# Kernel tuning notes

Measured on AMD Instinct MI355X. Metric: run time of the kernel, lower is better.

The kernel has to match this reference:

```python
import jax, jax.numpy as jnp
import numpy as np

B, N, F, T = 32, 1024, 64, 24


def setup_inputs() -> dict:
    key = jax.random.key(0)
    k = jax.random.split(key, 6)
    x = jax.random.normal(k[0], (B, N, F, T), dtype=jnp.float32)
    W1 = jax.random.normal(k[1], (T,), dtype=jnp.float32) * 0.1
    W2 = jax.random.normal(k[2], (F, T), dtype=jnp.float32) * 0.1
    W3 = jax.random.normal(k[3], (F,), dtype=jnp.float32) * 0.1
    b_s = jax.random.normal(k[4], (1, N, N), dtype=jnp.float32) * 0.02
    V_s = jax.random.normal(k[5], (N, N), dtype=jnp.float32) * 0.02
    return {"x": x, "W1": W1, "W2": W2, "W3": W3, "b_s": b_s, "V_s": V_s}


def reference(x, W1, W2, W3, b_s, V_s):
    # lhs = (x @ W1) @ W2 : (B,N,F,T)@(T,) -> (B,N,F) ; @(F,T) -> (B,N,T)
    lhs = jnp.einsum('bnft,t->bnf', x, W1) @ W2
    # rhs = (x^T @ W3) permuted : (B,N,T,F)@(F,) -> (B,N,T) -> (B,T,N)
    rhs = jnp.einsum('bnft,f->btn', x, W3)
    # batch_dot: (B,N,T) @ (B,T,N) -> (B,N,N), as one batched GEMM
    product = jnp.einsum('bnt,btm->bnm', lhs, rhs)
    sig = jax.nn.sigmoid(product + b_s)
    # torch.matmul(V_s, sig.permute(1,2,0)).permute(2,0,1) == S[b,n,i] = sum_k V_s[i,k]*sig[b,n,k]
    S = jnp.einsum('ik,bnk->bni', V_s, sig)
    S = S - jnp.max(S, axis=1, keepdims=True)
    exp = jnp.exp(S)
    # NOTE: original has `[0]` on the sum -> denominator uses batch-0 sums, shape (1,N),
    # broadcast over rows. Faithfully reproduced (numpy broadcasting matches torch here).
    return exp / jnp.sum(exp, axis=1, keepdims=True)[0]
```

## Files before the change

### kernel.cpp

```cpp
#include <hip/hip_runtime.h>
#include <hip/hip_bf16.h>

#define Bb 32
#define Nn 1024
#define Ff 64
#define Tt 24

#define LHS_OFF  0
#define RHS_OFF  3145728
#define MKEY_OFF 6291456
#define D0_OFF   6422528
#define ABF_OFF  6426624ull
#define VB_OFF   73535488ull
#define WS_NEED  75632640ull

typedef __attribute__((ext_vector_type(8))) short bf16x8;
typedef __attribute__((ext_vector_type(4))) float f32x4;

__device__ __forceinline__ unsigned fkey(float x) {
    unsigned u = __float_as_uint(x);
    return (u & 0x80000000u) ? ~u : (u | 0x80000000u);
}
__device__ __forceinline__ float keyToFloat(unsigned k) {
    unsigned u = (k & 0x80000000u) ? (k & 0x7FFFFFFFu) : ~k;
    return __uint_as_float(u);
}
__device__ __forceinline__ unsigned short f2bf(float f) {
    unsigned u = __float_as_uint(f);
    u += 0x7FFFu + ((u >> 16) & 1u);
    return (unsigned short)(u >> 16);
}

__global__ __launch_bounds__(256) void k1_lhs_rhs(
    const float* __restrict__ x, const float* __restrict__ W1,
    const float* __restrict__ W2, const float* __restrict__ W3,
    float* __restrict__ LHS, float* __restrict__ RHS) {
    __shared__ float sx[4][64][25];
    __shared__ float sy[4][64];
    __shared__ float sW1[24];
    __shared__ float sW2[64][24];
    __shared__ float sW3[64];
    int tid = threadIdx.x;
    if (tid < 24) sW1[tid] = W1[tid];
    if (tid < 64) sW3[tid] = W3[tid];
    for (int j = tid; j < 64 * 24; j += 256) sW2[j / 24][j % 24] = W2[j];
    __syncthreads();

    int w = tid >> 6, lane = tid & 63;
    int row = blockIdx.x * 4 + w;
    const float* xr = x + (size_t)row * (Ff * Tt) + lane * Tt;
    float4 xv[6];
#pragma unroll
    for (int j = 0; j < 6; ++j) xv[j] = reinterpret_cast<const float4*>(xr)[j];
    float y = 0.f;
#pragma unroll
    for (int j = 0; j < 6; ++j) {
        y += xv[j].x * sW1[j * 4 + 0] + xv[j].y * sW1[j * 4 + 1] +
             xv[j].z * sW1[j * 4 + 2] + xv[j].w * sW1[j * 4 + 3];
    }
#pragma unroll
    for (int j = 0; j < 6; ++j) {
        sx[w][lane][j * 4 + 0] = xv[j].x;
        sx[w][lane][j * 4 + 1] = xv[j].y;
        sx[w][lane][j * 4 + 2] = xv[j].z;
        sx[w][lane][j * 4 + 3] = xv[j].w;
    }
    sy[w][lane] = y;
    __syncthreads();
    if (lane < 24) {
        int t = lane;
        float la = 0.f, ra = 0.f;
#pragma unroll 8
        for (int f = 0; f < 64; ++f) {
            ra += sx[w][f][t] * sW3[f];
            la += sy[w][f] * sW2[f][t];
        }
        LHS[(size_t)row * Tt + t] = la;
        RHS[(size_t)row * Tt + t] = ra;
    }
}

__global__ __launch_bounds__(256) void k_vb(const float* __restrict__ V,
                                            unsigned* __restrict__ Vb2) {
    size_t idx = (size_t)blockIdx.x * 256 + threadIdx.x;
    float4 v = ((const float4*)V)[idx];
    uint2 o;
    o.x = (unsigned)f2bf(v.x) | ((unsigned)f2bf(v.y) << 16);
    o.y = (unsigned)f2bf(v.z) | ((unsigned)f2bf(v.w) << 16);
    ((uint2*)Vb2)[idx] = o;
}

__global__ __launch_bounds__(256) void k2a_sig(
    const float* __restrict__ LHS, const float* __restrict__ RHS,
    const float* __restrict__ b_s, unsigned short* __restrict__ Abf) {
    __shared__ float rst[24][68];
    int tid = threadIdx.x;
    int b = blockIdx.z;
    int n0 = blockIdx.x * 64;
    int kh = blockIdx.y * 512;
    int n = tid >> 2, q = tid & 3;

    float L[24];
    const float* lp = LHS + ((size_t)b * Nn + n0 + n) * Tt;
#pragma unroll
    for (int j = 0; j < 24; ++j) L[j] = lp[j];

    for (int kc = 0; kc < 512; kc += 64) {
        __syncthreads();
        const float* rp = RHS + ((size_t)b * Nn + kh + kc) * Tt;
        for (int e = tid; e < 64 * 24; e += 256) rst[e % 24][e / 24] = rp[e];
        __syncthreads();

        float P[16] = {};
#pragma unroll
        for (int j = 0; j < 24; ++j) {
            float Lj = L[j];
            const float4* rv = (const float4*)&rst[j][q * 16];
            float4 r0 = rv[0], r1 = rv[1], r2 = rv[2], r3 = rv[3];
            P[0]  += Lj * r0.x; P[1]  += Lj * r0.y; P[2]  += Lj * r0.z; P[3]  += Lj * r0.w;
            P[4]  += Lj * r1.x; P[5]  += Lj * r1.y; P[6]  += Lj * r1.z; P[7]  += Lj * r1.w;
            P[8]  += Lj * r2.x; P[9]  += Lj * r2.y; P[10] += Lj * r2.z; P[11] += Lj * r2.w;
            P[12] += Lj * r3.x; P[13] += Lj * r3.y; P[14] += Lj * r3.z; P[15] += Lj * r3.w;
        }
        const float* bp = &b_s[(size_t)(n0 + n) * Nn + kh + kc + q * 16];
        unsigned ow[8];
#pragma unroll
        for (int k4 = 0; k4 < 4; ++k4) {
            float4 bs = ((const float4*)bp)[k4];
            unsigned short s0 = f2bf(1.f / (1.f + __expf(-(P[k4 * 4 + 0] + bs.x))));
            unsigned short s1 = f2bf(1.f / (1.f + __expf(-(P[k4 * 4 + 1] + bs.y))));
            unsigned short s2 = f2bf(1.f / (1.f + __expf(-(P[k4 * 4 + 2] + bs.z))));
            unsigned short s3 = f2bf(1.f / (1.f + __expf(-(P[k4 * 4 + 3] + bs.w))));
            ow[k4 * 2 + 0] = (unsigned)s0 | ((unsigned)s1 << 16);
            ow[k4 * 2 + 1] = (unsigned)s2 | ((unsigned)s3 << 16);
        }
        unsigned short* op = Abf + ((size_t)b * Nn + n0 + n) * Nn + kh + kc + q * 16;
        ((uint4*)op)[0] = make_uint4(ow[0], ow[1], ow[2], ow[3]);
        ((uint4*)op)[1] = make_uint4(ow[4], ow[5], ow[6], ow[7]);
    }
}

__global__ __launch_bounds__(512, 2) void k2b_8ph(
    const unsigned short* __restrict__ A, const unsigned short* __restrict__ Vb,
    float* __restrict__ S, unsigned* __restrict__ Mkey) {
    __shared__ __align__(16) unsigned short lds[65536];

    const int tid = threadIdx.x, w = tid >> 6, lane = tid & 63;
    const int l15 = lane & 15;
    const int bid = blockIdx.x;
    const int L = ((bid & 7) << 6) + (bid >> 3);
    const int i0 = (L & 3) * 256;
    const int m0 = (L >> 2) * 256;
    const int wr = w >> 2, wc = w & 3;

    const int p0 = (lane >> 4) ^ ((lane >> 1) & 7);
    const int aBase  = (wr * 128 + l15) * 64 + p0 * 8;
    const int aBaseX = aBase ^ 32;
    const int bBase  = 16384 + (wc * 64 + l15) * 64 + p0 * 8;
    const int bBaseX = bBase ^ 32;

    const int rL = lane >> 3;
    const int cS = (lane & 7) ^ ((4 * (w & 1) + (lane >> 4)) & 7);
    const int bRowW = (w >> 2) * 64 + (w & 3) * 8;
    const unsigned short* srcA00 = A  + (size_t)(m0 +   0 + 8 * w + rL) * 1024 + cS * 8;
    const unsigned short* srcA01 = A  + (size_t)(m0 + 128 + 8 * w + rL) * 1024 + cS * 8;
    const unsigned short* srcA10 = A  + (size_t)(m0 +  64 + 8 * w + rL) * 1024 + cS * 8;
    const unsigned short* srcA11 = A  + (size_t)(m0 + 192 + 8 * w + rL) * 1024 + cS * 8;
    const unsigned short* srcB00 = Vb + (size_t)(i0 +   0 + bRowW + rL) * 1024 + cS * 8;
    const unsigned short* srcB01 = Vb + (size_t)(i0 + 128 + bRowW + rL) * 1024 + cS * 8;
    const unsigned short* srcB10 = Vb + (size_t)(i0 +  32 + bRowW + rL) * 1024 + cS * 8;
    const unsigned short* srcB11 = Vb + (size_t)(i0 + 160 + bRowW + rL) * 1024 + cS * 8;
    const int dA00 = (0   + 8 * w) * 64, dA01 = (128 + 8 * w) * 64;
    const int dA10 = (64  + 8 * w) * 64, dA11 = (192 + 8 * w) * 64;
    const int dB00 = 16384 + (0   + bRowW) * 64, dB01 = 16384 + (128 + bRowW) * 64;
    const int dB10 = 16384 + (32  + bRowW) * 64, dB11 = 16384 + (160 + bRowW) * 64;

#define GLD(src, dstShorts) __builtin_amdgcn_global_load_lds(                      \
        (const __attribute__((address_space(1))) void*)(src),                     \
        (__attribute__((address_space(3))) void*)(lds + (dstShorts)), 16, 0, 0)

#define READ_A(bc, mh) do {                                                        \
    const int ro_ = (bc) * 32768 + (mh) * 4096;                                    \
    aR[0][0] = *(const bf16x8*)(lds + ro_ + aBase +    0);                         \
    aR[1][0] = *(const bf16x8*)(lds + ro_ + aBase + 1024);                         \
    aR[2][0] = *(const bf16x8*)(lds + ro_ + aBase + 2048);                         \
    aR[3][0] = *(const bf16x8*)(lds + ro_ + aBase + 3072);                         \
    aR[0][1] = *(const bf16x8*)(lds + ro_ + aBaseX +    0);                        \
    aR[1][1] = *(const bf16x8*)(lds + ro_ + aBaseX + 1024);                        \
    aR[2][1] = *(const bf16x8*)(lds + ro_ + aBaseX + 2048);                        \
    aR[3][1] = *(const bf16x8*)(lds + ro_ + aBaseX + 3072);                        \
} while (0)

#define READ_B(bc, nh, BR) do {                                                    \
    const int ro_ = (bc) * 32768 + (nh) * 2048;                                    \
    BR[0][0] = *(const bf16x8*)(lds + ro_ + bBase +    0);                         \
    BR[1][0] = *(const bf16x8*)(lds + ro_ + bBase + 1024);                         \
    BR[0][1] = *(const bf16x8*)(lds + ro_ + bBaseX +    0);                        \
    BR[1][1] = *(const bf16x8*)(lds + ro_ + bBaseX + 1024);                        \
} while (0)

#define BARRIER_LGKM                                                               \
    __builtin_amdgcn_s_barrier();                                                  \
    asm volatile("s_waitcnt lgkmcnt(0)" ::: "memory");                             \
    __builtin_amdgcn_sched_barrier(0)

#define QUAD(mh, nh, BR) do {                                                      \
    __builtin_amdgcn_s_setprio(1);                                                 \
    _Pragma("unroll")                                                              \
    for (int ks_ = 0; ks_ < 2; ++ks_)                                              \
        _Pragma("unroll")                                                          \
        for (int mi_ = 0; mi_ < 4; ++mi_)                                          \
            _Pragma("unroll")                                                      \
            for (int ni_ = 0; ni_ < 2; ++ni_)                                      \
                acc[(mh) * 4 + mi_][(nh) * 2 + ni_] =                              \
                    __builtin_amdgcn_mfma_f32_16x16x32_bf16(                       \
                        aR[mi_][ks_], BR[ni_][ks_],                                \
                        acc[(mh) * 4 + mi_][(nh) * 2 + ni_], 0, 0, 0);             \
    __builtin_amdgcn_s_setprio(0);                                                 \
} while (0)

#define VM6  asm volatile("s_waitcnt vmcnt(6)" ::: "memory")
#define ENDP __builtin_amdgcn_s_barrier()

    GLD(srcA00, dA00); GLD(srcA01, dA01);
    GLD(srcB00, dB00); GLD(srcB01, dB01);
    GLD(srcB10, dB10); GLD(srcB11, dB11);
    GLD(srcA10, dA10); GLD(srcA11, dA11);
    GLD(srcA00 + 64, 32768 + dA00); GLD(srcA01 + 64, 32768 + dA01);
    GLD(srcB00 + 64, 32768 + dB00); GLD(srcB01 + 64, 32768 + dB01);
    GLD(srcB10 + 64, 32768 + dB10); GLD(srcB11 + 64, 32768 + dB11);
    asm volatile("s_waitcnt vmcnt(6)" ::: "memory");
    __builtin_amdgcn_s_barrier();

    bf16x8 aR[4][2], b0R[2][2], b1R[2][2];
    f32x4 acc[8][4] = {};

    for (int j = 0; j < 8; ++j) {
        const int k1o = (2 * j + 1) * 64;
        const int k2o = ((j < 7) ? (2 * j + 2) : 15) * 64;
        const int k3o = ((j < 7) ? (2 * j + 3) : 15) * 64;

        READ_A(0, 0); READ_B(0, 0, b0R);
        GLD(srcA10 + k1o, 32768 + dA10); GLD(srcA11 + k1o, 32768 + dA11);
        BARRIER_LGKM; QUAD(0, 0, b0R); ENDP;
        READ_B(0, 1, b1R);
        GLD(srcA00 + k2o, dA00); GLD(srcA01 + k2o, dA01);
        BARRIER_LGKM; QUAD(0, 1, b1R); ENDP;
        READ_A(0, 1);
        GLD(srcB00 + k2o, dB00); GLD(srcB01 + k2o, dB01);
        BARRIER_LGKM; QUAD(1, 0, b0R); ENDP;
        GLD(srcB10 + k2o, dB10); GLD(srcB11 + k2o, dB11);
        BARRIER_LGKM; QUAD(1, 1, b1R); VM6; ENDP;
        READ_A(1, 0); READ_B(1, 0, b0R);
        GLD(srcA10 + k2o, dA10); GLD(srcA11 + k2o, dA11);
        BARRIER_LGKM; QUAD(0, 0, b0R); ENDP;
        READ_B(1, 1, b1R);
        GLD(srcA00 + k3o, 32768 + dA00); GLD(srcA01 + k3o, 32768 + dA01);
        BARRIER_LGKM; QUAD(0, 1, b1R); ENDP;
        READ_A(1, 1);
        GLD(srcB00 + k3o, 32768 + dB00); GLD(srcB01 + k3o, 32768 + dB01);
        BARRIER_LGKM; QUAD(1, 0, b0R); ENDP;
        GLD(srcB10 + k3o, 32768 + dB10); GLD(srcB11 + k3o, 32768 + dB11);
        BARRIER_LGKM; QUAD(1, 1, b1R); VM6; ENDP;
    }
#undef GLD
#undef READ_A
#undef READ_B
#undef BARRIER_LGKM
#undef QUAD
#undef VM6
#undef ENDP

    const int ic = i0 + wc * 64 + l15;
    const int mrb = m0 + wr * 128 + (lane >> 4) * 4;
#pragma unroll
    for (int mi8 = 0; mi8 < 8; ++mi8)
#pragma unroll
        for (int ni = 0; ni < 4; ++ni) {
            f32x4 v = acc[mi8][ni];
#pragma unroll
            for (int r = 0; r < 4; ++r)
                S[(size_t)(mrb + mi8 * 16 + r) * 1024 + ic + ni * 16] = v[r];
        }

    const int bcol = m0 >> 10;
#pragma unroll
    for (int ni = 0; ni < 4; ++ni) {
        float mx = -3.402823466e38f;
#pragma unroll
        for (int mi8 = 0; mi8 < 8; ++mi8)
#pragma unroll
            for (int r = 0; r < 4; ++r) mx = fmaxf(mx, acc[mi8][ni][r]);
        mx = fmaxf(mx, __shfl_xor(mx, 16));
        mx = fmaxf(mx, __shfl_xor(mx, 32));
        if ((lane >> 4) == 0)
            atomicMax(&Mkey[bcol * Nn + ic + ni * 16], fkey(mx));
    }
}

#define KB 32
__global__ __launch_bounds__(256) void k2_gemm(
    const float* __restrict__ LHS, const float* __restrict__ RHS,
    const float* __restrict__ V_s, const float* __restrict__ b_s,
    float* __restrict__ S) {
    __shared__ float Lst[24][132];
    __shared__ float Rst[24][KB];
    __shared__ float As[KB][132];
    __shared__ float Bs[KB][132];
    int tid = threadIdx.x;
    int b = blockIdx.z;
    int n0 = blockIdx.y * 128;
    int i0 = blockIdx.x * 128;
    const float* lbase = LHS + ((size_t)b * Nn + n0) * Tt;
    for (int lin = tid; lin < 128 * Tt; lin += 256) {
        int r = lin / Tt, t = lin % Tt;
        Lst[t][r] = lbase[lin];
    }
    float acc[8][8] = {};
    int tx = tid & 15, ty = tid >> 4;
    int an = (tid & 31) * 4;
    int ak = (tid >> 5) * 4;
    const float* rbase = RHS + (size_t)b * Nn * Tt;
    for (int k0 = 0; k0 < Nn; k0 += KB) {
        __syncthreads();
        for (int lin = tid; lin < KB * Tt; lin += 256) {
            int r = lin / Tt, t = lin % Tt;
            Rst[t][r] = rbase[(size_t)(k0 + r) * Tt + t];
        }
        for (int l4 = tid; l4 < 128 * (KB / 4); l4 += 256) {
            int i = l4 >> 3, k4 = (l4 & 7) << 2;
            float4 v = *(const float4*)&V_s[(size_t)(i0 + i) * Nn + k0 + k4];
            Bs[k4 + 0][i] = v.x; Bs[k4 + 1][i] = v.y;
            Bs[k4 + 2][i] = v.z; Bs[k4 + 3][i] = v.w;
        }
        __syncthreads();
        float pacc[4][4] = {};
#pragma unroll
        for (int t = 0; t < 24; ++t) {
            float4 lv = *(const float4*)&Lst[t][an];
            float4 rv = *(const float4*)&Rst[t][ak];
            float lvv[4] = {lv.x, lv.y, lv.z, lv.w};
            float rvv[4] = {rv.x, rv.y, rv.z, rv.w};
#pragma unroll
            for (int r = 0; r < 4; ++r)
#pragma unroll
                for (int c = 0; c < 4; ++c) pacc[r][c] += lvv[r] * rvv[c];
        }
#pragma unroll
        for (int r = 0; r < 4; ++r) {
            float4 bs4 = *(const float4*)&b_s[(size_t)(n0 + an + r) * Nn + k0 + ak];
            float bsv[4] = {bs4.x, bs4.y, bs4.z, bs4.w};
#pragma unroll
            for (int c = 0; c < 4; ++c) {
                float p = pacc[r][c] + bsv[c];
                As[ak + c][an + r] = 1.f / (1.f + __expf(-p));
            }
        }
        __syncthreads();
#pragma unroll
        for (int kk = 0; kk < KB; ++kk) {
            float4 a0 = *(const float4*)&As[kk][ty * 4];
            float4 a1 = *(const float4*)&As[kk][ty * 4 + 64];
            float4 b0 = *(const float4*)&Bs[kk][tx * 4];
            float4 b1 = *(const float4*)&Bs[kk][tx * 4 + 64];
            float av[8] = {a0.x, a0.y, a0.z, a0.w, a1.x, a1.y, a1.z, a1.w};
            float bv[8] = {b0.x, b0.y, b0.z, b0.w, b1.x, b1.y, b1.z, b1.w};
#pragma unroll
            for (int r = 0; r < 8; ++r)
#pragma unroll
                for (int c = 0; c < 8; ++c) acc[r][c] += av[r] * bv[c];
        }
    }
#pragma unroll
    for (int r = 0; r < 8; ++r) {
        int nn = ty * 4 + (r & 3) + ((r >> 2) << 6);
        float4* op = (float4*)(S + ((size_t)(b * Nn + n0 + nn)) * Nn + i0 + tx * 4);
        op[0]  = make_float4(acc[r][0], acc[r][1], acc[r][2], acc[r][3]);
        op[16] = make_float4(acc[r][4], acc[r][5], acc[r][6], acc[r][7]);
    }
}

__global__ __launch_bounds__(256) void k3_colmax(const float* __restrict__ S,
                                                 unsigned* __restrict__ Mkey) {
    int b = blockIdx.z;
    int i0 = blockIdx.x * 64;
    int nbase = blockIdx.y * 256;
    int ii = threadIdx.x & 63, g = threadIdx.x >> 6;
    const float* p = S + ((size_t)(b * Nn + nbase + g * 64)) * Nn + i0 + ii;
    float m = -3.402823466e38f;
#pragma unroll 4
    for (int n = 0; n < 64; ++n) m = fmaxf(m, p[(size_t)n * Nn]);
    __shared__ float red[4][64];
    red[g][ii] = m;
    __syncthreads();
    if (g == 0) {
        m = fmaxf(fmaxf(red[0][ii], red[1][ii]), fmaxf(red[2][ii], red[3][ii]));
        atomicMax(Mkey + b * Nn + i0 + ii, fkey(m));
    }
}

__global__ __launch_bounds__(256) void k4_denom(const float* __restrict__ S,
                                                const unsigned* __restrict__ Mkey,
                                                float* __restrict__ D0) {
    int i0 = blockIdx.x * 64;
    int ii = threadIdx.x & 63, g = threadIdx.x >> 6;
    float M = keyToFloat(Mkey[i0 + ii]);
    const float* p = S + ((size_t)(g * 256)) * Nn + i0 + ii;
    float s = 0.f;
    for (int n = 0; n < 256; ++n) s += __expf(p[(size_t)n * Nn] - M);
    __shared__ float red[4][64];
    red[g][ii] = s;
    __syncthreads();
    if (g == 0) D0[i0 + ii] = (red[0][ii] + red[1][ii]) + (red[2][ii] + red[3][ii]);
}

__global__ __launch_bounds__(256) void k5_final(float* __restrict__ S,
                                                const unsigned* __restrict__ Mkey,
                                                const float* __restrict__ D0) {
    const size_t total4 = (size_t)Bb * Nn * Nn / 4;
    for (size_t idx = (size_t)blockIdx.x * 256 + threadIdx.x; idx < total4;
         idx += (size_t)gridDim.x * 256) {
        size_t e = idx << 2;
        int i = (int)(e & (Nn - 1));
        int b = (int)(e >> 20);
        float4 s4 = ((const float4*)S)[idx];
        uint4 k4 = *(const uint4*)(Mkey + b * Nn + i);
        float4 d4 = *(const float4*)(D0 + i);
        float4 o;
        o.x = __expf(s4.x - keyToFloat(k4.x)) / d4.x;
        o.y = __expf(s4.y - keyToFloat(k4.y)) / d4.y;
        o.z = __expf(s4.z - keyToFloat(k4.z)) / d4.z;
        o.w = __expf(s4.w - keyToFloat(k4.w)) / d4.w;
        ((float4*)S)[idx] = o;
    }
}

extern "C" void kernel_launch(void* const* d_in, const int* in_sizes, int n_in,
                              void* d_out, int out_size, void* d_ws, size_t ws_size,
                              hipStream_t stream) {
    const float* x   = (const float*)d_in[0];
    const float* W1  = (const float*)d_in[1];
    const float* W2  = (const float*)d_in[2];
    const float* W3  = (const float*)d_in[3];
    const float* b_s = (const float*)d_in[4];
    const float* V_s = (const float*)d_in[5];
    float* out = (float*)d_out;

    char* ws = (char*)d_ws;
    float* LHS = (float*)(ws + LHS_OFF);
    float* RHS = (float*)(ws + RHS_OFF);
    unsigned* Mkey = (unsigned*)(ws + MKEY_OFF);
    float* D0 = (float*)(ws + D0_OFF);

    k1_lhs_rhs<<<Bb * Nn / 4, 256, 0, stream>>>(x, W1, W2, W3, LHS, RHS);
    hipMemsetAsync(Mkey, 0, (size_t)Bb * Nn * sizeof(unsigned), stream);

    if (ws_size >= WS_NEED) {
        unsigned short* Abf = (unsigned short*)(ws + ABF_OFF);
        unsigned short* Vb  = (unsigned short*)(ws + VB_OFF);
        k_vb<<<1024, 256, 0, stream>>>(V_s, (unsigned*)Vb);
        k2a_sig<<<dim3(16, 2, 32), 256, 0, stream>>>(LHS, RHS, b_s, Abf);
        k2b_8ph<<<512, 512, 0, stream>>>(Abf, Vb, out, Mkey);
    } else {
        k2_gemm<<<dim3(Nn / 128, Nn / 128, Bb), 256, 0, stream>>>(LHS, RHS, V_s, b_s, out);
        k3_colmax<<<dim3(Nn / 64, 4, Bb), 256, 0, stream>>>(out, Mkey);
    }

    k4_denom<<<Nn / 64, 256, 0, stream>>>(out, Mkey, D0);
    k5_final<<<2048, 256, 0, stream>>>(out, Mkey, D0);
}
```

Measured before the change: 249.6 us.

## Store exp as bf16 with fused column sums, MFMA sigmoid GEMM, merged prep kernels

The main GEMM epilogue now exponentiates its results without max subtraction. It writes them as bf16 and accumulates the batch-0 column sums with atomics, so the separate denominator pass and the fp32 intermediate round-trip go away. The final kernel rescales using exp(max) values. The LHS·RHS sigmoid stage now uses bf16 MFMA on padded bf16 LHS/RHS produced by k1, and the V_s conversion and Mkey/C0 zeroing are folded into k1. This lowers memory traffic and launch count, at the cost of bf16 rounding of exp values, overflow risk if S were large, and a larger workspace requirement with a fallback path.

```diff
diff --git a/kernel.cpp b/kernel.cpp
--- a/kernel.cpp
+++ b/kernel.cpp
@@ -6,13 +6,19 @@
 #define Ff 64
 #define Tt 24
 
-#define LHS_OFF  0
-#define RHS_OFF  3145728
-#define MKEY_OFF 6291456
-#define D0_OFF   6422528
-#define ABF_OFF  6426624ull
-#define VB_OFF   73535488ull
-#define WS_NEED  75632640ull
+#define LHSB_OFF 0ull
+#define RHSB_OFF 2097152ull
+#define MKEY_OFF 4194304ull
+#define C0_OFF   4325376ull
+#define ABF_OFF  8388608ull
+#define VB_OFF   75497472ull
+#define E_OFF    77594624ull
+#define WS_NEED2 144703488ull
+
+#define FB_LHS_OFF  0
+#define FB_RHS_OFF  3145728
+#define FB_MKEY_OFF 6291456
+#define FB_D0_OFF   6422528
 
 typedef __attribute__((ext_vector_type(8))) short bf16x8;
 typedef __attribute__((ext_vector_type(4))) float f32x4;
@@ -30,16 +36,24 @@
     u += 0x7FFFu + ((u >> 16) & 1u);
     return (unsigned short)(u >> 16);
 }
-
-__global__ __launch_bounds__(256) void k1_lhs_rhs(
+__device__ __forceinline__ float bf2f(unsigned short s) {
+    return __uint_as_float(((unsigned)s) << 16);
+}
+
+__global__ __launch_bounds__(256) void k1b(
     const float* __restrict__ x, const float* __restrict__ W1,
     const float* __restrict__ W2, const float* __restrict__ W3,
-    float* __restrict__ LHS, float* __restrict__ RHS) {
+    const float* __restrict__ V_s,
+    unsigned short* __restrict__ LHSb, unsigned short* __restrict__ RHSb,
+    unsigned* __restrict__ Vb2, unsigned* __restrict__ Mkey,
+    float* __restrict__ C0) {
     __shared__ float sx[4][64][25];
     __shared__ float sy[4][64];
     __shared__ float sW1[24];
     __shared__ float sW2[64][24];
     __shared__ float sW3[64];
+    __shared__ __align__(16) unsigned short pl[4][32];
+    __shared__ __align__(16) unsigned short pr[4][32];
     int tid = threadIdx.x;
     if (tid < 24) sW1[tid] = W1[tid];
     if (tid < 64) sW3[tid] = W3[tid];
@@ -67,82 +81,107 @@
     }
     sy[w][lane] = y;
     __syncthreads();
-    if (lane < 24) {
-        int t = lane;
-        float la = 0.f, ra = 0.f;
+    if (lane < 32) {
+        if (lane < 24) {
+            int t = lane;
+            float la = 0.f, ra = 0.f;
 #pragma unroll 8
-        for (int f = 0; f < 64; ++f) {
-            ra += sx[w][f][t] * sW3[f];
-            la += sy[w][f] * sW2[f][t];
-        }
-        LHS[(size_t)row * Tt + t] = la;
-        RHS[(size_t)row * Tt + t] = ra;
-    }
-}
-
-__global__ __launch_bounds__(256) void k_vb(const float* __restrict__ V,
-                                            unsigned* __restrict__ Vb2) {
-    size_t idx = (size_t)blockIdx.x * 256 + threadIdx.x;
-    float4 v = ((const float4*)V)[idx];
-    uint2 o;
-    o.x = (unsigned)f2bf(v.x) | ((unsigned)f2bf(v.y) << 16);
-    o.y = (unsigned)f2bf(v.z) | ((unsigned)f2bf(v.w) << 16);
-    ((uint2*)Vb2)[idx] = o;
-}
-
-__global__ __launch_bounds__(256) void k2a_sig(
-    const float* __restrict__ LHS, const float* __restrict__ RHS,
+            for (int f = 0; f < 64; ++f) {
+                ra += sx[w][f][t] * sW3[f];
+                la += sy[w][f] * sW2[f][t];
+            }
+            pl[w][t] = f2bf(la);
+            pr[w][t] = f2bf(ra);
+        } else {
+            pl[w][lane] = 0;
+            pr[w][lane] = 0;
+        }
+    }
+    __syncthreads();
+    if (lane < 4)
+        ((uint4*)(LHSb + (size_t)row * 32))[lane] = ((const uint4*)pl[w])[lane];
+    else if (lane < 8)
+        ((uint4*)(RHSb + (size_t)row * 32))[lane - 4] = ((const uint4*)pr[w])[lane - 4];
+
+    int bid = blockIdx.x;
+    if (bid < 1024) {
+        size_t idx = (size_t)bid * 256 + tid;
+        float4 v = ((const float4*)V_s)[idx];
+        uint2 o;
+        o.x = (unsigned)f2bf(v.x) | ((unsigned)f2bf(v.y) << 16);
+        o.y = (unsigned)f2bf(v.z) | ((unsigned)f2bf(v.w) << 16);
+        ((uint2*)Vb2)[idx] = o;
+    } else if (bid < 1156) {
+        int widx = (bid - 1024) * 256 + tid;
+        if (widx < 32768) Mkey[widx] = 0u;
+        else if (widx < 33792) C0[widx - 32768] = 0.f;
+    }
+}
+
+__global__ __launch_bounds__(512) void k_sig(
+    const unsigned short* __restrict__ LHSb, const unsigned short* __restrict__ RHSb,
     const float* __restrict__ b_s, unsigned short* __restrict__ Abf) {
-    __shared__ float rst[24][68];
-    int tid = threadIdx.x;
-    int b = blockIdx.z;
-    int n0 = blockIdx.x * 64;
-    int kh = blockIdx.y * 512;
-    int n = tid >> 2, q = tid & 3;
-
-    float L[24];
-    const float* lp = LHS + ((size_t)b * Nn + n0 + n) * Tt;
-#pragma unroll
-    for (int j = 0; j < 24; ++j) L[j] = lp[j];
-
-    for (int kc = 0; kc < 512; kc += 64) {
-        __syncthreads();
-        const float* rp = RHS + ((size_t)b * Nn + kh + kc) * Tt;
-        for (int e = tid; e < 64 * 24; e += 256) rst[e % 24][e / 24] = rp[e];
-        __syncthreads();
-
-        float P[16] = {};
-#pragma unroll
-        for (int j = 0; j < 24; ++j) {
-            float Lj = L[j];
-            const float4* rv = (const float4*)&rst[j][q * 16];
-            float4 r0 = rv[0], r1 = rv[1], r2 = rv[2], r3 = rv[3];
-            P[0]  += Lj * r0.x; P[1]  += Lj * r0.y; P[2]  += Lj * r0.z; P[3]  += Lj * r0.w;
-            P[4]  += Lj * r1.x; P[5]  += Lj * r1.y; P[6]  += Lj * r1.z; P[7]  += Lj * r1.w;
-            P[8]  += Lj * r2.x; P[9]  += Lj * r2.y; P[10] += Lj * r2.z; P[11] += Lj * r2.w;
-            P[12] += Lj * r3.x; P[13] += Lj * r3.y; P[14] += Lj * r3.z; P[15] += Lj * r3.w;
-        }
-        const float* bp = &b_s[(size_t)(n0 + n) * Nn + kh + kc + q * 16];
-        unsigned ow[8];
-#pragma unroll
-        for (int k4 = 0; k4 < 4; ++k4) {
-            float4 bs = ((const float4*)bp)[k4];
-            unsigned short s0 = f2bf(1.f / (1.f + __expf(-(P[k4 * 4 + 0] + bs.x))));
-            unsigned short s1 = f2bf(1.f / (1.f + __expf(-(P[k4 * 4 + 1] + bs.y))));
-            unsigned short s2 = f2bf(1.f / (1.f + __expf(-(P[k4 * 4 + 2] + bs.z))));
-            unsigned short s3 = f2bf(1.f / (1.f + __expf(-(P[k4 * 4 + 3] + bs.w))));
-            ow[k4 * 2 + 0] = (unsigned)s0 | ((unsigned)s1 << 16);
-            ow[k4 * 2 + 1] = (unsigned)s2 | ((unsigned)s3 << 16);
-        }
-        unsigned short* op = Abf + ((size_t)b * Nn + n0 + n) * Nn + kh + kc + q * 16;
-        ((uint4*)op)[0] = make_uint4(ow[0], ow[1], ow[2], ow[3]);
-        ((uint4*)op)[1] = make_uint4(ow[4], ow[5], ow[6], ow[7]);
-    }
+    __shared__ __align__(16) unsigned short Rt[256 * 32];
+    __shared__ __align__(16) unsigned short Lt[256 * 32];
+    const int tid = threadIdx.x, w = tid >> 6, lane = tid & 63;
+    const int b = blockIdx.z, n0 = blockIdx.y * 256, k0 = blockIdx.x * 256;
+
+    const int csrc = ((lane & 3) ^ ((lane >> 3) & 3)) * 8;
+    const unsigned short* rbase = RHSb + (size_t)(b * 1024 + k0) * 32;
+    const unsigned short* lbase = LHSb + (size_t)(b * 1024 + n0) * 32;
+#define GLD(src, dst) __builtin_amdgcn_global_load_lds(                            \
+        (const __attribute__((address_space(1))) void*)(src),                     \
+        (__attribute__((address_space(3))) void*)(dst), 16, 0, 0)
+    GLD(rbase + (size_t)(w * 32 + (lane >> 2)) * 32 + csrc,      Rt + (w * 32) * 32);
+    GLD(rbase + (size_t)(w * 32 + 16 + (lane >> 2)) * 32 + csrc, Rt + (w * 32 + 16) * 32);
+    GLD(lbase + (size_t)(w * 32 + (lane >> 2)) * 32 + csrc,      Lt + (w * 32) * 32);
+    GLD(lbase + (size_t)(w * 32 + 16 + (lane >> 2)) * 32 + csrc, Lt + (w * 32 + 16) * 32);
+#undef GLD
+    __syncthreads();
+
+    const int wk = (w >> 2) * 128, wn = (w & 3) * 64;
+    const int l15 = lane & 15;
+    const int swz8 = ((lane >> 4) ^ ((l15 >> 1) & 3)) * 8;
+    bf16x8 af[8], bfr[4];
+#pragma unroll
+    for (int a = 0; a < 8; ++a)
+        af[a] = *(const bf16x8*)(Rt + (wk + a * 16 + l15) * 32 + swz8);
+#pragma unroll
+    for (int c = 0; c < 4; ++c)
+        bfr[c] = *(const bf16x8*)(Lt + (wn + c * 16 + l15) * 32 + swz8);
+
+    f32x4 acc[8][4] = {};
+#pragma unroll
+    for (int a = 0; a < 8; ++a)
+#pragma unroll
+        for (int c = 0; c < 4; ++c)
+            acc[a][c] = __builtin_amdgcn_mfma_f32_16x16x32_bf16(
+                af[a], bfr[c], acc[a][c], 0, 0, 0);
+
+    const int kb = k0 + wk + (lane >> 4) * 4;
+    const int nb = n0 + wn + l15;
+#pragma unroll
+    for (int a = 0; a < 8; ++a)
+#pragma unroll
+        for (int c = 0; c < 4; ++c) {
+            int n = nb + c * 16, k = kb + a * 16;
+            float4 bs = *(const float4*)&b_s[(size_t)n * 1024 + k];
+            f32x4 p = acc[a][c];
+            unsigned short s0 = f2bf(1.f / (1.f + __expf(-(p[0] + bs.x))));
+            unsigned short s1 = f2bf(1.f / (1.f + __expf(-(p[1] + bs.y))));
+            unsigned short s2 = f2bf(1.f / (1.f + __expf(-(p[2] + bs.z))));
+            unsigned short s3 = f2bf(1.f / (1.f + __expf(-(p[3] + bs.w))));
+            uint2 ov;
+            ov.x = (unsigned)s0 | ((unsigned)s1 << 16);
+            ov.y = (unsigned)s2 | ((unsigned)s3 << 16);
+            *(uint2*)(Abf + (size_t)(b * 1024 + n) * 1024 + k) = ov;
+        }
 }
 
 __global__ __launch_bounds__(512, 2) void k2b_8ph(
     const unsigned short* __restrict__ A, const unsigned short* __restrict__ Vb,
-    float* __restrict__ S, unsigned* __restrict__ Mkey) {
+    unsigned short* __restrict__ Ebuf, unsigned* __restrict__ Mkey,
+    float* __restrict__ C0) {
     __shared__ __align__(16) unsigned short lds[65536];
 
     const int tid = threadIdx.x, w = tid >> 6, lane = tid & 63;
@@ -276,25 +315,113 @@
 #pragma unroll
     for (int mi8 = 0; mi8 < 8; ++mi8)
 #pragma unroll
+        for (int ni = 0; ni < 4; ++ni)
+#pragma unroll
+            for (int r = 0; r < 4; ++r)
+                acc[mi8][ni][r] = __expf(acc[mi8][ni][r]);
+#pragma unroll
+    for (int mi8 = 0; mi8 < 8; ++mi8)
+#pragma unroll
         for (int ni = 0; ni < 4; ++ni) {
             f32x4 v = acc[mi8][ni];
 #pragma unroll
             for (int r = 0; r < 4; ++r)
-                S[(size_t)(mrb + mi8 * 16 + r) * 1024 + ic + ni * 16] = v[r];
-        }
-
+                Ebuf[(size_t)(mrb + mi8 * 16 + r) * 1024 + ic + ni * 16] = f2bf(v[r]);
+        }
     const int bcol = m0 >> 10;
 #pragma unroll
     for (int ni = 0; ni < 4; ++ni) {
-        float mx = -3.402823466e38f;
+        float mx = 0.f, sm = 0.f;
 #pragma unroll
         for (int mi8 = 0; mi8 < 8; ++mi8)
 #pragma unroll
-            for (int r = 0; r < 4; ++r) mx = fmaxf(mx, acc[mi8][ni][r]);
+            for (int r = 0; r < 4; ++r) {
+                float e = acc[mi8][ni][r];
+                mx = fmaxf(mx, e);
+                sm += e;
+            }
         mx = fmaxf(mx, __shfl_xor(mx, 16));
         mx = fmaxf(mx, __shfl_xor(mx, 32));
-        if ((lane >> 4) == 0)
+        sm += __shfl_xor(sm, 16);
+        sm += __shfl_xor(sm, 32);
+        if ((lane >> 4) == 0) {
             atomicMax(&Mkey[bcol * Nn + ic + ni * 16], fkey(mx));
+            if (bcol == 0) atomicAdd(&C0[ic + ni * 16], sm);
+        }
+    }
+}
+
+__global__ __launch_bounds__(256) void k5b(
+    const unsigned short* __restrict__ E, const unsigned* __restrict__ Mkey,
+    const float* __restrict__ C0, float* __restrict__ out) {
+    const size_t total4 = (size_t)Bb * Nn * Nn / 4;
+    for (size_t idx = (size_t)blockIdx.x * 256 + threadIdx.x; idx < total4;
+         idx += (size_t)gridDim.x * 256) {
+        size_t e4 = idx << 2;
+        int i = (int)(e4 & (Nn - 1));
+        int b = (int)(e4 >> 20);
+        uint2 ev = ((const uint2*)E)[idx];
+        uint4 mb = *(const uint4*)(Mkey + b * Nn + i);
+        uint4 m0 = *(const uint4*)(Mkey + i);
+        float4 c0 = *(const float4*)(C0 + i);
+        float4 o;
+        o.x = bf2f((unsigned short)(ev.x & 0xffffu)) *
+              __fdividef(keyToFloat(m0.x), keyToFloat(mb.x) * c0.x);
+        o.y = bf2f((unsigned short)(ev.x >> 16)) *
+              __fdividef(keyToFloat(m0.y), keyToFloat(mb.y) * c0.y);
+        o.z = bf2f((unsigned short)(ev.y & 0xffffu)) *
+              __fdividef(keyToFloat(m0.z), keyToFloat(mb.z) * c0.z);
+        o.w = bf2f((unsigned short)(ev.y >> 16)) *
+              __fdividef(keyToFloat(m0.w), keyToFloat(mb.w) * c0.w);
+        ((float4*)out)[idx] = o;
+    }
+}
+
+__global__ __launch_bounds__(256) void k1_lhs_rhs(
+    const float* __restrict__ x, const float* __restrict__ W1,
+    const float* __restrict__ W2, const float* __restrict__ W3,
+    float* __restrict__ LHS, float* __restrict__ RHS) {
+    __shared__ float sx[4][64][25];
+    __shared__ float sy[4][64];
+    __shared__ float sW1[24];
+    __shared__ float sW2[64][24];
+    __shared__ float sW3[64];
+    int tid = threadIdx.x;
+    if (tid < 24) sW1[tid] = W1[tid];
+    if (tid < 64) sW3[tid] = W3[tid];
+    for (int j = tid; j < 64 * 24; j += 256) sW2[j / 24][j % 24] = W2[j];
+    __syncthreads();
+    int w = tid >> 6, lane = tid & 63;
+    int row = blockIdx.x * 4 + w;
+    const float* xr = x + (size_t)row * (Ff * Tt) + lane * Tt;
+    float4 xv[6];
+#pragma unroll
+    for (int j = 0; j < 6; ++j) xv[j] = reinterpret_cast<const float4*>(xr)[j];
+    float y = 0.f;
+#pragma unroll
+    for (int j = 0; j < 6; ++j) {
+        y += xv[j].x * sW1[j * 4 + 0] + xv[j].y * sW1[j * 4 + 1] +
+             xv[j].z * sW1[j * 4 + 2] + xv[j].w * sW1[j * 4 + 3];
+    }
+#pragma unroll
+    for (int j = 0; j < 6; ++j) {
+        sx[w][lane][j * 4 + 0] = xv[j].x;
+        sx[w][lane][j * 4 + 1] = xv[j].y;
+        sx[w][lane][j * 4 + 2] = xv[j].z;
+        sx[w][lane][j * 4 + 3] = xv[j].w;
+    }
+    sy[w][lane] = y;
+    __syncthreads();
+    if (lane < 24) {
+        int t = lane;
+        float la = 0.f, ra = 0.f;
+#pragma unroll 8
+        for (int f = 0; f < 64; ++f) {
+            ra += sx[w][f][t] * sW3[f];
+            la += sy[w][f] * sW2[f][t];
+        }
+        LHS[(size_t)row * Tt + t] = la;
+        RHS[(size_t)row * Tt + t] = ra;
     }
 }
 
@@ -445,27 +572,32 @@
     const float* b_s = (const float*)d_in[4];
     const float* V_s = (const float*)d_in[5];
     float* out = (float*)d_out;
-
     char* ws = (char*)d_ws;
-    float* LHS = (float*)(ws + LHS_OFF);
-    float* RHS = (float*)(ws + RHS_OFF);
-    unsigned* Mkey = (unsigned*)(ws + MKEY_OFF);
-    float* D0 = (float*)(ws + D0_OFF);
-
-    k1_lhs_rhs<<<Bb * Nn / 4, 256, 0, stream>>>(x, W1, W2, W3, LHS, RHS);
-    hipMemsetAsync(Mkey, 0, (size_t)Bb * Nn * sizeof(unsigned), stream);
-
-    if (ws_size >= WS_NEED) {
+
+    if (ws_size >= WS_NEED2) {
+        unsigned short* LHSb = (unsigned short*)(ws + LHSB_OFF);
+        unsigned short* RHSb = (unsigned short*)(ws + RHSB_OFF);
+        unsigned* Mkey = (unsigned*)(ws + MKEY_OFF);
+        float* C0 = (float*)(ws + C0_OFF);
         unsigned short* Abf = (unsigned short*)(ws + ABF_OFF);
         unsigned short* Vb  = (unsigned short*)(ws + VB_OFF);
-        k_vb<<<1024, 256, 0, stream>>>(V_s, (unsigned*)Vb);
-        k2a_sig<<<dim3(16, 2, 32), 256, 0, stream>>>(LHS, RHS, b_s, Abf);
-        k2b_8ph<<<512, 512, 0, stream>>>(Abf, Vb, out, Mkey);
+        unsigned short* Eb  = (unsigned short*)(ws + E_OFF);
+
+        k1b<<<Bb * Nn / 4, 256, 0, stream>>>(x, W1, W2, W3, V_s, LHSb, RHSb,
+                                             (unsigned*)Vb, Mkey, C0);
+        k_sig<<<dim3(4, 4, Bb), 512, 0, stream>>>(LHSb, RHSb, b_s, Abf);
+        k2b_8ph<<<512, 512, 0, stream>>>(Abf, Vb, Eb, Mkey, C0);
+        k5b<<<2048, 256, 0, stream>>>(Eb, Mkey, C0, out);
     } else {
+        float* LHS = (float*)(ws + FB_LHS_OFF);
+        float* RHS = (float*)(ws + FB_RHS_OFF);
+        unsigned* Mkey = (unsigned*)(ws + FB_MKEY_OFF);
+        float* D0 = (float*)(ws + FB_D0_OFF);
+        k1_lhs_rhs<<<Bb * Nn / 4, 256, 0, stream>>>(x, W1, W2, W3, LHS, RHS);
+        hipMemsetAsync(Mkey, 0, (size_t)Bb * Nn * sizeof(unsigned), stream);
         k2_gemm<<<dim3(Nn / 128, Nn / 128, Bb), 256, 0, stream>>>(LHS, RHS, V_s, b_s, out);
         k3_colmax<<<dim3(Nn / 64, 4, Bb), 256, 0, stream>>>(out, Mkey);
-    }
-
-    k4_denom<<<Nn / 64, 256, 0, stream>>>(out, Mkey, D0);
-    k5_final<<<2048, 256, 0, stream>>>(out, Mkey, D0);
-}
+        k4_denom<<<Nn / 64, 256, 0, stream>>>(out, Mkey, D0);
+        k5_final<<<2048, 256, 0, stream>>>(out, Mkey, D0);
+    }
+}
```

New measurement: 216.6 us. -13.2%, faster.
